# Kernel tuning notes

Measured on AMD Instinct MI355X. Metric: run time of the kernel, lower is better.

The kernel has to match this reference:

```python
import jax, jax.numpy as jnp
import numpy as np

XBAR = 128            # XBAR_ROW_SIZE == XBAR_COL_SIZE (PUMA crossbar)
WB, WF = 16, 12       # weight_bits, weight_bit_frac
IB, IF = 16, 12       # input_bits, input_bit_frac
BIT_SLICE, NSLICE = 2, 8      # weight_bits // bit_slice slices per weight
BIT_STREAM, NSTREAM = 1, 16   # input_bits // bit_stream streams
ADC_BIT = 9           # log2(128) + bit_slice
ACM_BITS, ACM_FRAC = 16, 12
STRIDE, PAD, K = 1, 1, 3


def setup_inputs() -> dict:
    key = jax.random.key(0)
    k1, k2 = jax.random.split(key)
    x = jax.random.normal(k1, (4, 64, 16, 16), jnp.float32)
    # modest weight scale so the 16-bit accumulator (range ~ +/-8) is not saturated
    w = 0.05 * jax.random.normal(k2, (128, 64, 3, 3), jnp.float32)
    return {"x": x, "w": w}


def _extract_patches(xpad, k, stride):
    # xpad: [B, C, Hp, Wp] -> [B, OH*OW, C*k*k] with (c, ki, kj) channel order (== torch unfold)
    B, C, Hp, Wp = xpad.shape
    OH = (Hp - k) // stride + 1
    OW = (Wp - k) // stride + 1
    cols = []
    for ki in range(k):
        for kj in range(k):
            cols.append(xpad[:, :, ki:ki + OH * stride:stride, kj:kj + OW * stride:stride])
    p = jnp.stack(cols, axis=2)                      # [B, C, k*k, OH, OW]
    return p.reshape(B, C * k * k, OH * OW).transpose(0, 2, 1), OH, OW


def _bit_slice_weights(w_mag):
    # w_mag [Cout, L] nonneg -> padded crossbar matrix [Lp, Cout*NSLICE], MSB slice first
    Cout, L = w_mag.shape
    w_int = jnp.clip(jnp.round(w_mag * (1 << WF)), 0, (1 << WB) - 1).astype(jnp.int32)
    shifts = (BIT_SLICE * jnp.arange(NSLICE - 1, -1, -1)).astype(jnp.int32)
    slices = (w_int[..., None] >> shifts) & ((1 << BIT_SLICE) - 1)   # [Cout, L, NSLICE]
    mat = slices.transpose(1, 0, 2).reshape(L, Cout * NSLICE).astype(jnp.float32)
    Lp = -(-L // XBAR) * XBAR
    return jnp.pad(mat, ((0, Lp - L), (0, 0)))


def _mvm(bits, Wm):
    # bits [P, R, XBAR, T] binary streams; Wm [R, XBAR, J] conductance slices.
    # Per-crossbar analog column sums -> ADC quantize -> shift-add slices & streams.
    analog = jnp.einsum('prkt,rkj->prjt', bits, Wm)
    adc = jnp.clip(jnp.round(analog), 0.0, float((1 << ADC_BIT) - 1))
    P, R, J, T = adc.shape
    adc = adc.reshape(P, R, J // NSLICE, NSLICE, T)
    sl_w = (2.0 ** (BIT_SLICE * jnp.arange(NSLICE - 1, -1, -1))).astype(jnp.float32)
    st_w = (2.0 ** jnp.arange(NSTREAM)).astype(jnp.float32)
    st_w = st_w.at[-1].multiply(-1.0)   # two's-complement sign bit (bit_stream == 1 path)
    return jnp.einsum('prcst,s,t->pc', adc, sl_w, st_w)   # sums over crossbar rows too


def mvm_conv(x, w):
    B, Cin, H, W = x.shape
    Cout = w.shape[0]
    xpad = jnp.pad(x, ((0, 0), (0, 0), (PAD, PAD), (PAD, PAD)))
    patches, OH, OW = _extract_patches(xpad, K, STRIDE)
    L = Cin * K * K
    P = B * OH * OW
    v = patches.reshape(P, L)
    # input fixed point -> 16-bit two's complement bit streams, LSB first
    x_int = jnp.round(v * (1 << IF)).astype(jnp.int32)
    x_u = x_int & ((1 << IB) - 1)
    bits = ((x_u[..., None] >> jnp.arange(IB, dtype=jnp.int32)) & 1).astype(jnp.float32)
    Lp = -(-L // XBAR) * XBAR
    bits = jnp.pad(bits, ((0, 0), (0, Lp - L), (0, 0))).reshape(P, Lp // XBAR, XBAR, NSTREAM)
    wf = w.reshape(Cout, L)
    Wpos = _bit_slice_weights(jnp.clip(wf, 0.0, None)).reshape(Lp // XBAR, XBAR, Cout * NSLICE)
    Wneg = _bit_slice_weights(jnp.abs(jnp.clip(wf, None, 0.0))).reshape(Lp // XBAR, XBAR, Cout * NSLICE)
    out = (_mvm(bits, Wpos) - _mvm(bits, Wneg)) / float(1 << (WF + IF))
    # accumulator fixed-point quantization (acm_bits / acm_bit_frac)
    scale = float(1 << ACM_FRAC)
    lo, hi = float(-(1 << (ACM_BITS - 1))), float((1 << (ACM_BITS - 1)) - 1)
    out = jnp.clip(jnp.round(out * scale), lo, hi) / scale
    return out.reshape(B, OH, OW, Cout).transpose(0, 3, 1, 2)


def reference(x, w):
    return mvm_conv(x, w)
```

## Files before the change

kernel.cpp:

```cpp
#include <hip/hip_runtime.h>


#define CIN 64
#define COUT 128
#define HW 16
#define LDIM 576
#define LP 288
#define QS 4096.0f
#define CC 32
#define PXT 16

typedef short short2v __attribute__((ext_vector_type(2)));

__device__ inline int dot2(int a, int b, int c) {
#if __has_builtin(__builtin_amdgcn_sdot2)
    union { int i; short2v v; } ua, ub;
    ua.i = a; ub.i = b;
    return __builtin_amdgcn_sdot2(ua.v, ub.v, c, false);
#else
    return c + (int)(short)(a & 0xFFFF) * (int)(short)(b & 0xFFFF)
             + (a >> 16) * (b >> 16);
#endif
}

__device__ inline int pack16(int s0, int s1) {
    return (int)(((unsigned)(unsigned short)(short)s1 << 16) |
                 (unsigned short)(short)s0);
}

__global__ __launch_bounds__(256) void fused_conv_kernel(const float* __restrict__ x,
                                                         const float* __restrict__ w,
                                                         float* __restrict__ out) {
    __shared__ int ws2[144 * 64];
    __shared__ int xs[PXT][LP];

    const int tid = threadIdx.x;
    const int ctile = blockIdx.x & 3;
    const int pxtile = blockIdx.x >> 2;
    const int c0 = ctile * CC;
    const int b  = pxtile >> 4;
    const int oh = pxtile & 15;

    {
        const int cc = tid & 31, kb = tid >> 5;
        const float4* w4 = (const float4*)w;
        #pragma unroll
        for (int k = 0; k < 18; ++k) {
            int lp2 = kb + k * 8;
            float4 wv = w4[(c0 + cc) * 144 + lp2];
            int i0 = (int)rintf(wv.x * QS);
            int i1 = (int)rintf(wv.y * QS);
            int i2 = (int)rintf(wv.z * QS);
            int i3 = (int)rintf(wv.w * QS);
            ((int2*)ws2)[lp2 * 32 + cc] = make_int2(pack16(i0, i1), pack16(i2, i3));
        }
    }

    {
        const int px = tid >> 4;
        const int j  = tid & 15;
        #pragma unroll 2
        for (int t = 0; t < 18; ++t) {
            int lp = j * 18 + t;
            int s[2];
            #pragma unroll
            for (int u = 0; u < 2; ++u) {
                int l = lp * 2 + u;
                int cin = l / 9, r = l - cin * 9, ki = r / 3, kj = r - ki * 3;
                int ih = oh - 1 + ki, iw = px - 1 + kj;
                float v = 0.0f;
                if ((unsigned)ih < HW && (unsigned)iw < HW)
                    v = x[((b * CIN + cin) * HW + ih) * HW + iw];
                s[u] = (int)rintf(v * QS);
            }
            xs[px][lp] = pack16(s[0], s[1]);
        }
    }
    __syncthreads();

    const int c  = tid & 31;
    const int pp = tid >> 5;
    const int4* xA = (const int4*)xs[2 * pp];
    const int4* xB = (const int4*)xs[2 * pp + 1];
    const int2* wp = (const int2*)ws2;
    int acc0 = 0, acc1 = 0;
    #pragma unroll 8
    for (int q = 0; q < 72; ++q) {
        int4 xa = xA[q], xb = xB[q];
        int2 wA = wp[(2 * q) * 32 + c];
        int2 wB = wp[(2 * q + 1) * 32 + c];
        acc0 = dot2(xa.x, wA.x, dot2(xa.y, wA.y, dot2(xa.z, wB.x, dot2(xa.w, wB.y, acc0))));
        acc1 = dot2(xb.x, wA.x, dot2(xb.y, wA.y, dot2(xb.z, wB.x, dot2(xb.w, wB.y, acc1))));
    }

    int accs[2] = {acc0, acc1};
    float o[2];
    #pragma unroll
    for (int jj = 0; jj < 2; ++jj) {
        int a = accs[jj];
        int f = a >> 12, r = a & 4095;
        int q = f + ((r > 2048) || (r == 2048 && (f & 1)));
        q = min(max(q, -32768), 32767);
        o[jj] = (float)q * (1.0f / QS);
    }
    float2* o2 = (float2*)&out[(((b * COUT + c0 + c) * HW + oh) * HW) + 2 * pp];
    *o2 = make_float2(o[0], o[1]);
}

extern "C" void kernel_launch(void* const* d_in, const int* in_sizes, int n_in,
                              void* d_out, int out_size, void* d_ws, size_t ws_size,
                              hipStream_t stream) {
    const float* x = (const float*)d_in[0];
    const float* w = (const float*)d_in[1];
    float* out = (float*)d_out;
    fused_conv_kernel<<<256, 256, 0, stream>>>(x, w, out);
}
```

Baseline: 68.13 us.

## Stage input halo tile instead of im2col and retile blocks over 4 channels

```diff
diff --git a/kernel.cpp b/kernel.cpp
--- a/kernel.cpp
+++ b/kernel.cpp
@@ -4,11 +4,7 @@
 #define CIN 64
 #define COUT 128
 #define HW 16
-#define LDIM 576
-#define LP 288
 #define QS 4096.0f
-#define CC 32
-#define PXT 16
 
 typedef short short2v __attribute__((ext_vector_type(2)));
 
@@ -31,80 +27,71 @@
 __global__ __launch_bounds__(256) void fused_conv_kernel(const float* __restrict__ x,
                                                          const float* __restrict__ w,
                                                          float* __restrict__ out) {
-    __shared__ int ws2[144 * 64];
-    __shared__ int xs[PXT][LP];
+    __shared__ int   xs[108 * 32];
+    __shared__ short wsh[4][9][64];
 
     const int tid = threadIdx.x;
-    const int ctile = blockIdx.x & 3;
-    const int pxtile = blockIdx.x >> 2;
-    const int c0 = ctile * CC;
-    const int b  = pxtile >> 4;
-    const int oh = pxtile & 15;
+    const int ct = blockIdx.x & 31;
+    const int pt = blockIdx.x >> 5;
+    const int c0 = ct * 4;
+    const int b  = pt >> 2;
+    const int oh0 = (pt & 3) * 4;
 
-    {
-        const int cc = tid & 31, kb = tid >> 5;
-        const float4* w4 = (const float4*)w;
+    for (int i = tid; i < 576; i += 256) {
+        int cc = i / 144, q = i - cc * 144;
+        float4 wv = ((const float4*)w)[(c0 + cc) * 144 + q];
+        float f[4] = {wv.x, wv.y, wv.z, wv.w};
         #pragma unroll
-        for (int k = 0; k < 18; ++k) {
-            int lp2 = kb + k * 8;
-            float4 wv = w4[(c0 + cc) * 144 + lp2];
-            int i0 = (int)rintf(wv.x * QS);
-            int i1 = (int)rintf(wv.y * QS);
-            int i2 = (int)rintf(wv.z * QS);
-            int i3 = (int)rintf(wv.w * QS);
-            ((int2*)ws2)[lp2 * 32 + cc] = make_int2(pack16(i0, i1), pack16(i2, i3));
+        for (int u = 0; u < 4; ++u) {
+            int lu = q * 4 + u;
+            int cin = lu / 9, kk = lu - cin * 9;
+            wsh[cc][kk][cin] = (short)(int)rintf(f[u] * QS);
         }
     }
 
-    {
-        const int px = tid >> 4;
-        const int j  = tid & 15;
-        #pragma unroll 2
-        for (int t = 0; t < 18; ++t) {
-            int lp = j * 18 + t;
-            int s[2];
-            #pragma unroll
-            for (int u = 0; u < 2; ++u) {
-                int l = lp * 2 + u;
-                int cin = l / 9, r = l - cin * 9, ki = r / 3, kj = r - ki * 3;
-                int ih = oh - 1 + ki, iw = px - 1 + kj;
-                float v = 0.0f;
-                if ((unsigned)ih < HW && (unsigned)iw < HW)
-                    v = x[((b * CIN + cin) * HW + ih) * HW + iw];
-                s[u] = (int)rintf(v * QS);
-            }
-            xs[px][lp] = pack16(s[0], s[1]);
+    for (int i = tid; i < 3456; i += 256) {
+        int cin2 = i / 108, pos = i - cin2 * 108;
+        int ih6 = pos / 18, iws = pos - ih6 * 18;
+        int ih = oh0 - 1 + ih6, iw = iws - 1;
+        int s0 = 0, s1 = 0;
+        if ((unsigned)ih < HW && (unsigned)iw < HW) {
+            const float* xp = &x[((b * CIN + 2 * cin2) * HW + ih) * HW + iw];
+            s0 = (int)rintf(xp[0] * QS);
+            s1 = (int)rintf(xp[HW * HW] * QS);
         }
+        int ch = cin2 >> 2;
+        xs[pos * 32 + ((ch ^ (pos & 7)) << 2) + (cin2 & 3)] = pack16(s0, s1);
     }
     __syncthreads();
 
-    const int c  = tid & 31;
-    const int pp = tid >> 5;
-    const int4* xA = (const int4*)xs[2 * pp];
-    const int4* xB = (const int4*)xs[2 * pp + 1];
-    const int2* wp = (const int2*)ws2;
-    int acc0 = 0, acc1 = 0;
-    #pragma unroll 8
-    for (int q = 0; q < 72; ++q) {
-        int4 xa = xA[q], xb = xB[q];
-        int2 wA = wp[(2 * q) * 32 + c];
-        int2 wB = wp[(2 * q + 1) * 32 + c];
-        acc0 = dot2(xa.x, wA.x, dot2(xa.y, wA.y, dot2(xa.z, wB.x, dot2(xa.w, wB.y, acc0))));
-        acc1 = dot2(xb.x, wA.x, dot2(xb.y, wA.y, dot2(xb.z, wB.x, dot2(xb.w, wB.y, acc1))));
+    const int cc   = tid >> 6;
+    const int lane = tid & 63;
+    const int ohr  = lane >> 4, ow = lane & 15;
+    int acc0 = 0, acc1 = 0, acc2 = 0, acc3 = 0;
+    #pragma unroll
+    for (int ki = 0; ki < 3; ++ki) {
+        #pragma unroll
+        for (int kj = 0; kj < 3; ++kj) {
+            int pos  = (ohr + ki) * 18 + ow + kj;
+            int base = pos * 32, p7 = pos & 7;
+            const int4* wrow = (const int4*)&wsh[cc][ki * 3 + kj][0];
+            #pragma unroll
+            for (int ch = 0; ch < 8; ++ch) {
+                int4 xa = *(const int4*)&xs[base + ((ch ^ p7) << 2)];
+                int4 wa = wrow[ch];
+                acc0 = dot2(xa.x, wa.x, acc0);
+                acc1 = dot2(xa.y, wa.y, acc1);
+                acc2 = dot2(xa.z, wa.z, acc2);
+                acc3 = dot2(xa.w, wa.w, acc3);
+            }
+        }
     }
 
-    int accs[2] = {acc0, acc1};
-    float o[2];
-    #pragma unroll
-    for (int jj = 0; jj < 2; ++jj) {
-        int a = accs[jj];
-        int f = a >> 12, r = a & 4095;
-        int q = f + ((r > 2048) || (r == 2048 && (f & 1)));
-        q = min(max(q, -32768), 32767);
-        o[jj] = (float)q * (1.0f / QS);
-    }
-    float2* o2 = (float2*)&out[(((b * COUT + c0 + c) * HW + oh) * HW) + 2 * pp];
-    *o2 = make_float2(o[0], o[1]);
+    int a = acc0 + acc1 + acc2 + acc3;
+    int fl = a >> 12, r = a & 4095;
+    int q = fl + ((r > 2048) || (r == 2048 && (fl & 1)));
+    q = min(max(q, -32768), 32767);
+    out[((b * COUT + c0 + cc) * HW + oh0 + ohr) * HW + ow] = (float)q * (1.0f / QS);
 }
 
 extern "C" void kernel_launch(void* const* d_in, const int* in_sizes, int n_in,
@@ -113,5 +100,5 @@
     const float* x = (const float*)d_in[0];
     const float* w = (const float*)d_in[1];
     float* out = (float*)d_out;
-    fused_conv_kernel<<<256, 256, 0, stream>>>(x, w, out);
+    fused_conv_kernel<<<512, 256, 0, stream>>>(x, w, out);
 }
```

Result: faster. 63.99 us (-6.1%).
